# Optimization experiments

Hardware: AMD Instinct MI355X
Metric: run time of the kernel (lower is better)

The kernel has to match this reference:

```python
import jax, jax.numpy as jnp
import numpy as np

V, E, HT, HC = 30000, 300, 256, 256
B, LC, T = 32, 32, 64
NTAG = 9  # output_dim + 2


def lstm_dir(x, lens, Wih, Whh, b, reverse):
    """Variable-length single-direction LSTM (packed-sequence semantics).
    x: [N, T, D], lens: [N] int. Returns outputs [N, T, H] zeroed at pad steps.
    Masked state update keeps h,c frozen at pad steps, so reverse=True starts
    from each sequence's true last element (zeros carry through leading pads).
    """
    N, Tn, _ = x.shape
    H = Whh.shape[1]
    gx = jnp.einsum('ntd,gd->ntg', x, Wih) + b            # [N,T,4H]
    mask = jnp.arange(Tn)[None, :] < lens[:, None]         # [N,T]

    def step(carry, inp):
        h, c = carry
        g_t, m = inp                                       # [N,4H], [N]
        gates = g_t + h @ Whh.T
        i, f, g, o = jnp.split(gates, 4, axis=-1)
        c_new = jax.nn.sigmoid(f) * c + jax.nn.sigmoid(i) * jnp.tanh(g)
        h_new = jax.nn.sigmoid(o) * jnp.tanh(c_new)
        m = m[:, None]
        h2 = jnp.where(m, h_new, h)
        c2 = jnp.where(m, c_new, c)
        return (h2, c2), jnp.where(m, h2, 0.0)

    init = (jnp.zeros((N, H), x.dtype), jnp.zeros((N, H), x.dtype))
    xs = (jnp.swapaxes(gx, 0, 1), mask.T)
    _, ys = jax.lax.scan(step, init, xs, reverse=reverse)
    return jnp.swapaxes(ys, 0, 1)                          # [N,T,H]


def bilstm(x, lens, Wih_f, Whh_f, b_f, Wih_b, Whh_b, b_b):
    hf = lstm_dir(x, lens, Wih_f, Whh_f, b_f, reverse=False)
    hb = lstm_dir(x, lens, Wih_b, Whh_b, b_b, reverse=True)
    return jnp.concatenate([hf, hb], axis=-1)


def setup_inputs() -> dict:
    key = jax.random.key(0)
    ks = jax.random.split(key, 20)
    s = 0.05
    inp = {
        'x': jax.random.randint(ks[0], (B, LC, T), 0, V, dtype=jnp.int32),
        'x_feats': jax.random.normal(ks[1], (B, LC, 64), jnp.float32),
        'x_len': jnp.maximum(jax.random.randint(ks[2], (B,), 0, LC, dtype=jnp.int32), 1),
        'x_chunk_len': jax.random.randint(ks[3], (B, LC), 1, T + 1, dtype=jnp.int32),
        'emb': jax.random.normal(ks[4], (V, E), jnp.float32) * s,
        'tok_Wih_f': jax.random.normal(ks[5], (4 * HT, E), jnp.float32) * s,
        'tok_Whh_f': jax.random.normal(ks[6], (4 * HT, HT), jnp.float32) * s,
        'tok_b_f': jax.random.normal(ks[7], (4 * HT,), jnp.float32) * s,
        'tok_Wih_b': jax.random.normal(ks[8], (4 * HT, E), jnp.float32) * s,
        'tok_Whh_b': jax.random.normal(ks[9], (4 * HT, HT), jnp.float32) * s,
        'tok_b_b': jax.random.normal(ks[10], (4 * HT,), jnp.float32) * s,
        'chk_Wih_f': jax.random.normal(ks[11], (4 * HC, 2 * HT), jnp.float32) * s,
        'chk_Whh_f': jax.random.normal(ks[12], (4 * HC, HC), jnp.float32) * s,
        'chk_b_f': jax.random.normal(ks[13], (4 * HC,), jnp.float32) * s,
        'chk_Wih_b': jax.random.normal(ks[14], (4 * HC, 2 * HT), jnp.float32) * s,
        'chk_Whh_b': jax.random.normal(ks[15], (4 * HC, HC), jnp.float32) * s,
        'chk_b_b': jax.random.normal(ks[16], (4 * HC,), jnp.float32) * s,
        'fc_W': jax.random.normal(ks[17], (NTAG, 2 * HC), jnp.float32) * s,
        'fc_b': jax.random.normal(ks[18], (NTAG,), jnp.float32) * s,
    }
    return inp


def reference(x, x_feats, x_len, x_chunk_len, emb,
              tok_Wih_f, tok_Whh_f, tok_b_f, tok_Wih_b, tok_Whh_b, tok_b_b,
              chk_Wih_f, chk_Whh_f, chk_b_f, chk_Wih_b, chk_Whh_b, chk_b_b,
              fc_W, fc_b):
    b, lc, t = x.shape
    xe = emb[x].reshape(b * lc, t, -1)                     # [B*LC, T, E]
    clens = jnp.clip(x_chunk_len.reshape(-1), 1, t)        # [B*LC]
    h = bilstm(xe, clens, tok_Wih_f, tok_Whh_f, tok_b_f,
               tok_Wih_b, tok_Whh_b, tok_b_b)              # [B*LC, T, 2HT]
    # gather output at last valid timestep (= [fwd final, bwd one-step])
    last = h[jnp.arange(b * lc), clens - 1]                # [B*LC, 2HT]
    chunks = last.reshape(b, lc, -1)                       # [B, LC, 2HT]
    ch = bilstm(chunks, x_len, chk_Wih_f, chk_Whh_f, chk_b_f,
                chk_Wih_b, chk_Whh_b, chk_b_b)             # [B, LC, 2HC]
    # pad_packed(total_length=LC) gives zeros at pad -> fc sees zeros there
    out = ch @ fc_W.T + fc_b                               # [B, LC, NTAG]
    return out
```

## Files before the change

### kernel.cpp

```cpp
#include <hip/hip_runtime.h>


typedef __attribute__((ext_vector_type(8))) short s16x8;
typedef __attribute__((ext_vector_type(4))) float f32x4;
typedef __attribute__((ext_vector_type(2))) unsigned int u32x2;
typedef __attribute__((ext_vector_type(4))) unsigned int u32x4;

__device__ __forceinline__ unsigned short f2bf(float f) {
  unsigned u = __builtin_bit_cast(unsigned, f);
  u += 0x7fff + ((u >> 16) & 1);
  return (unsigned short)(u >> 16);
}
__device__ __forceinline__ float bf2f(unsigned short h) {
  unsigned u = ((unsigned)h) << 16;
  return __builtin_bit_cast(float, u);
}
__device__ __forceinline__ float sigm(float x) { return 1.f / (1.f + __expf(-x)); }
__device__ __forceinline__ float tanh_(float x) { return 1.f - 2.f / (__expf(2.f * x) + 1.f); }

union PK8 { s16x8 v; unsigned short u[8]; };

__global__ void prep_weights(const float* __restrict__ wihf, const float* __restrict__ wihb,
                             const float* __restrict__ wcf, const float* __restrict__ wcb,
                             unsigned short* __restrict__ o_wf, unsigned short* __restrict__ o_wb,
                             unsigned short* __restrict__ o_wcf, unsigned short* __restrict__ o_wcb) {
  const int job = blockIdx.y, r = blockIdx.x, tid = threadIdx.x;
  const float* src; unsigned short* dst; int Ks, Kd;
  switch (job) {
    case 0: src = wihf; dst = o_wf;   Ks = 300; Kd = 320; break;
    case 1: src = wihb; dst = o_wb;   Ks = 300; Kd = 320; break;
    case 2: src = wcf;  dst = o_wcf;  Ks = 512; Kd = 512; break;
    default:src = wcb;  dst = o_wcb;  Ks = 512; Kd = 512; break;
  }
  for (int c = tid; c < Kd; c += 256)
    dst[r * Kd + c] = f2bf(c < Ks ? src[r * Ks + c] : 0.f);
}

__global__ __launch_bounds__(256)
void prep_whh_frag(const float* __restrict__ w0, const float* __restrict__ w1,
                   const float* __restrict__ w2,
                   unsigned short* __restrict__ o0, unsigned short* __restrict__ o1,
                   unsigned short* __restrict__ o2) {
  const float* src = blockIdx.y == 0 ? w0 : (blockIdx.y == 1 ? w1 : w2);
  unsigned short* dst = blockIdx.y == 0 ? o0 : (blockIdx.y == 1 ? o1 : o2);
  const int fid = blockIdx.x;
  const int b = fid & 1, g = (fid >> 1) & 3, kt = (fid >> 3) & 7, js = fid >> 6;
  for (int i = threadIdx.x; i < 512; i += 256) {
    const int lane = i >> 3, e = i & 7;
    const int cc = lane & 15, qq = lane >> 4;
    const int row = g * 256 + (js * 2 + b) * 16 + cc;
    const int col = kt * 32 + qq * 8 + e;
    dst[(size_t)fid * 512 + i] = f2bf(src[row * 256 + col]);
  }
}

__global__ void prep_small(const int* __restrict__ x, const int* __restrict__ xcl,
                           int* __restrict__ clens, int* __restrict__ lastv,
                           int* __restrict__ order, int* __restrict__ glen) {
  __shared__ int start[65];
  const int n = threadIdx.x;
  if (n < 65) start[n] = 0;
  __syncthreads();
  int len = xcl[n]; len = len < 1 ? 1 : (len > 64 ? 64 : len);
  clens[n] = len;
  lastv[n] = x[n * 64 + len - 1];
  atomicAdd(&start[len], 1);
  __syncthreads();
  if (n == 0) {
    int acc = 0;
    for (int l = 64; l >= 1; --l) { int h = start[l]; start[l] = acc; acc += h; }
  }
  __syncthreads();
  int pos = atomicAdd(&start[len], 1);
  order[pos] = n;
  __syncthreads();
  if (n < 64) glen[n] = clens[order[n * 16]];
}

__global__ __launch_bounds__(256, 2)
void gemm_bf(const float* __restrict__ A, const int* __restrict__ rowmap,
             int Mrows, int Astride, int Klog, int KP,
             const unsigned short* __restrict__ B, unsigned short* __restrict__ C) {
  __shared__ unsigned short As[128 * 40];
  __shared__ unsigned short Ep[4][64 * 136];
  const int tid = threadIdx.x;
  const int lane = tid & 63, w = tid >> 6;
  const int wrow = w >> 1, wcol = w & 1;
  const int cc = lane & 15, qq = lane >> 4;
  const int m0 = blockIdx.y * 128, n0 = blockIdx.x * 256;

  f32x4 zz = {0.f, 0.f, 0.f, 0.f};
  f32x4 acc[4][8];
#pragma unroll
  for (int i = 0; i < 4; ++i)
#pragma unroll
    for (int j = 0; j < 8; ++j) acc[i][j] = zz;

  const int arow = tid >> 1, ahalf = tid & 1;
  const float* arp = nullptr;
  {
    int av = m0 + arow;
    if (av < Mrows) {
      int amap = rowmap ? rowmap[av] : av;
      arp = A + (long)amap * Astride;
    }
  }

  const int nktiles = KP >> 5;
  for (int kt = 0; kt < nktiles; ++kt) {
    const int k0 = kt << 5;
    __syncthreads();
    {
      const int kb = k0 + ahalf * 16;
      unsigned short hv[16];
      if (arp && kb + 16 <= Klog) {
        const float* p = arp + kb;
#pragma unroll
        for (int i = 0; i < 16; i += 4) {
          f32x4 t = *(const f32x4*)(p + i);
          hv[i] = f2bf(t.x); hv[i + 1] = f2bf(t.y);
          hv[i + 2] = f2bf(t.z); hv[i + 3] = f2bf(t.w);
        }
      } else {
#pragma unroll
        for (int i = 0; i < 16; ++i) {
          float v = (arp && (kb + i) < Klog) ? arp[kb + i] : 0.f;
          hv[i] = f2bf(v);
        }
      }
      PK8 p0, p1;
#pragma unroll
      for (int i = 0; i < 8; ++i) { p0.u[i] = hv[i]; p1.u[i] = hv[8 + i]; }
      *(s16x8*)&As[arow * 40 + ahalf * 16] = p0.v;
      *(s16x8*)&As[arow * 40 + ahalf * 16 + 8] = p1.v;
    }
    __syncthreads();
    s16x8 af[4];
#pragma unroll
    for (int mt = 0; mt < 4; ++mt)
      af[mt] = *(const s16x8*)&As[(wrow * 64 + mt * 16 + cc) * 40 + qq * 8];
#pragma unroll
    for (int nt = 0; nt < 8; ++nt) {
      const unsigned short* bp = B + (long)(n0 + wcol * 128 + nt * 16 + cc) * KP + k0 + qq * 8;
      s16x8 bfr = *(const s16x8*)bp;
#pragma unroll
      for (int mt = 0; mt < 4; ++mt)
        acc[mt][nt] = __builtin_amdgcn_mfma_f32_16x16x32_bf16(af[mt], bfr, acc[mt][nt], 0, 0, 0);
    }
  }
  __syncthreads();
#pragma unroll
  for (int mt = 0; mt < 4; ++mt)
#pragma unroll
    for (int nt = 0; nt < 8; ++nt)
#pragma unroll
      for (int r = 0; r < 4; ++r)
        Ep[w][(mt * 16 + qq * 4 + r) * 136 + nt * 16 + cc] = f2bf(acc[mt][nt][r]);
  __syncthreads();
#pragma unroll
  for (int it = 0; it < 16; ++it) {
    int row = it * 4 + qq;
    s16x8 d = *(const s16x8*)&Ep[w][row * 136 + cc * 8];
    int gm = m0 + wrow * 64 + row;
    int gn = n0 + wcol * 128 + cc * 8;
    if (gm < Mrows) *(s16x8*)&C[(long)gm * 1024 + gn] = d;
  }
}

__global__ void bwd_step(const unsigned short* __restrict__ gxb,
                         const float* __restrict__ bias,
                         float* __restrict__ chunks) {
  const int n = blockIdx.x, j = threadIdx.x;
  const unsigned short* row = gxb + (long)n * 1024;
  float gi = bf2f(row[j]) + bias[j];
  float gg = bf2f(row[512 + j]) + bias[512 + j];
  float go = bf2f(row[768 + j]) + bias[768 + j];
  float cn = sigm(gi) * tanh_(gg);
  chunks[(long)n * 512 + 256 + j] = sigm(go) * tanh_(cn);
}

__device__ __forceinline__ int gx_perm(int j) {
  return (j & ~31) + ((j & 15) << 1) + ((j >> 4) & 1);
}

__global__ __launch_bounds__(256)
void gather_gx(const unsigned short* __restrict__ proj, const int* __restrict__ x,
               const int* __restrict__ order, const int* __restrict__ clens,
               const int* __restrict__ glen, const float* __restrict__ bias,
               unsigned short* __restrict__ gx) {
  const int t = blockIdx.x, p = blockIdx.y, j = threadIdx.x;
  if (t >= glen[p >> 4]) return;
  const int seq = order[p];
  const int len = clens[seq];
  if (t >= len) return;
  unsigned short* dst = gx + (((size_t)(p >> 4) * 64 + t) * 16 + (p & 15)) * 1024 + gx_perm(j) * 4;
  const int tok = x[seq * 64 + t];
  const unsigned short* src = proj + (size_t)tok * 1024 + j;
  unsigned v0 = f2bf(bf2f(src[0]) + bias[j]);
  unsigned v1 = f2bf(bf2f(src[256]) + bias[256 + j]);
  unsigned v2 = f2bf(bf2f(src[512]) + bias[512 + j]);
  unsigned v3 = f2bf(bf2f(src[768]) + bias[768 + j]);
  u32x2 pk = {v0 | (v1 << 16), v2 | (v3 << 16)};
  *(u32x2*)dst = pk;
}

__global__ __launch_bounds__(256)
void repack4(const unsigned short* __restrict__ s0, const unsigned short* __restrict__ s1,
             const float* __restrict__ b0, const float* __restrict__ b1,
             unsigned short* __restrict__ d0, unsigned short* __restrict__ d1) {
  const int r = blockIdx.x, j = threadIdx.x;
  const int m = r >> 5, t = r & 31;
  const int mg = m >> 4, m16 = m & 15;
  const unsigned short* s = (blockIdx.y ? s1 : s0) + (size_t)r * 1024;
  const float* bb = blockIdx.y ? b1 : b0;
  unsigned short* d = (blockIdx.y ? d1 : d0) +
                      (size_t)((mg * 32 + t) * 16 + m16) * 1024 + gx_perm(j) * 4;
  unsigned v0 = f2bf(bf2f(s[j]) + bb[j]);
  unsigned v1 = f2bf(bf2f(s[256 + j]) + bb[256 + j]);
  unsigned v2 = f2bf(bf2f(s[512 + j]) + bb[512 + j]);
  unsigned v3 = f2bf(bf2f(s[768 + j]) + bb[768 + j]);
  u32x2 pk = {v0 | (v1 << 16), v2 | (v3 << 16)};
  *(u32x2*)d = pk;
}

__global__ __launch_bounds__(512, 2)
void tok_fwd(const unsigned short* __restrict__ gx,
             const unsigned short* __restrict__ WhP,
             const int* __restrict__ order,
             const int* __restrict__ clens,
             const int* __restrict__ glen,
             float* __restrict__ chunks) {
  extern __shared__ unsigned short smem[];
  unsigned short* hbuf = smem;
  unsigned short* ldsW = smem + 8448;
  int* sg = (int*)(smem + 8448 + 65536);
  int* slen = sg + 16;

  const int tid = threadIdx.x;
  const int lane = tid & 63, w = tid >> 6;
  const int cc = lane & 15, qq = lane >> 4;
  const int gb = blockIdx.x;

  if (tid < 16) {
    int s = order[gb * 16 + tid];
    sg[tid] = s;
    slen[tid] = clens[s];
  }
  for (int i = tid; i < 4224; i += 512) hbuf[i] = 0;

  const unsigned short* wgl = WhP + (size_t)w * 64 * 512 + lane * 8;
  {
    unsigned short* ld = ldsW + w * 8192 + lane * 8;
#pragma unroll
    for (int s = 0; s < 16; ++s)
      *(s16x8*)&ld[s * 512] = *(const s16x8*)&wgl[s * 512];
  }
  s16x8 Rw[40];
#pragma unroll
  for (int s = 0; s < 40; ++s)
    Rw[s] = *(const s16x8*)&wgl[(16 + s) * 512];

  __syncthreads();

  const int maxlen = glen[gb];
  int lenr[4];
#pragma unroll
  for (int r = 0; r < 4; ++r) lenr[r] = slen[qq * 4 + r];

  float cst[8];
  unsigned short hreg[8];
#pragma unroll
  for (int i = 0; i < 8; ++i) { cst[i] = 0.f; hreg[i] = 0; }

  const int j0 = w * 32 + cc;
  const unsigned short* gx0 = gx + (size_t)gb * 64 * 16 * 1024 + (w * 32 + cc * 2) * 4;
  const unsigned short* ldw = ldsW + w * 8192 + lane * 8;
  f32x4 zz = {0.f, 0.f, 0.f, 0.f};

  for (int t = 0; t < maxlen; ++t) {
    const unsigned short* hr = hbuf + (t & 1) * 4224;
    unsigned short* hw = hbuf + ((t & 1) ^ 1) * 4224;

    __syncthreads();

    s16x8 W7[4];
#pragma unroll
    for (int s = 0; s < 4; ++s)
      W7[s] = *(const s16x8*)&wgl[(56 + s) * 512];

    u32x4 gxp[4];
#pragma unroll
    for (int r = 0; r < 4; ++r)
      gxp[r] = *(const u32x4*)(gx0 + ((size_t)t * 16 + qq * 4 + r) * 1024);

    f32x4 acc[8];
#pragma unroll
    for (int s = 0; s < 8; ++s) acc[s] = zz;

#pragma unroll
    for (int kt = 0; kt < 2; ++kt) {
      s16x8 a0 = *(const s16x8*)&hr[cc * 264 + kt * 32 + qq * 8];
#pragma unroll
      for (int s = 0; s < 8; ++s)
        acc[s] = __builtin_amdgcn_mfma_f32_16x16x32_bf16(
            a0, *(const s16x8*)&ldw[(kt * 8 + s) * 512], acc[s], 0, 0, 0);
    }
#pragma unroll
    for (int kt = 2; kt < 7; ++kt) {
      s16x8 a0 = *(const s16x8*)&hr[cc * 264 + kt * 32 + qq * 8];
#pragma unroll
      for (int s = 0; s < 8; ++s)
        acc[s] = __builtin_amdgcn_mfma_f32_16x16x32_bf16(
            a0, Rw[(kt - 2) * 8 + s], acc[s], 0, 0, 0);
    }
    {
      s16x8 a7 = *(const s16x8*)&hr[cc * 264 + 7 * 32 + qq * 8];
#pragma unroll
      for (int s = 0; s < 4; ++s)
        acc[s] = __builtin_amdgcn_mfma_f32_16x16x32_bf16(a7, W7[s], acc[s], 0, 0, 0);
#pragma unroll
      for (int s = 0; s < 4; ++s)
        W7[s] = *(const s16x8*)&wgl[(60 + s) * 512];
#pragma unroll
      for (int s = 0; s < 4; ++s)
        acc[4 + s] = __builtin_amdgcn_mfma_f32_16x16x32_bf16(a7, W7[s], acc[4 + s], 0, 0, 0);
    }

#pragma unroll
    for (int r = 0; r < 4; ++r) {
      const int m = qq * 4 + r;
      const bool upd = t < lenr[r];
      const u32x4 pk = gxp[r];
#pragma unroll
      for (int jj = 0; jj < 2; ++jj) {
        const unsigned lo = jj ? pk.z : pk.x;
        const unsigned hi = jj ? pk.w : pk.y;
        float gi = acc[0 * 2 + jj][r] + bf2f((unsigned short)(lo & 0xffff));
        float gf = acc[1 * 2 + jj][r] + bf2f((unsigned short)(lo >> 16));
        float gg = acc[2 * 2 + jj][r] + bf2f((unsigned short)(hi & 0xffff));
        float go = acc[3 * 2 + jj][r] + bf2f((unsigned short)(hi >> 16));
        const int si = r * 2 + jj;
        if (upd) {
          float cn = sigm(gf) * cst[si] + sigm(gi) * tanh_(gg);
          cst[si] = cn;
          hreg[si] = f2bf(sigm(go) * tanh_(cn));
        }
        hw[m * 264 + j0 + jj * 16] = hreg[si];
      }
    }
  }

#pragma unroll
  for (int r = 0; r < 4; ++r)
#pragma unroll
    for (int jj = 0; jj < 2; ++jj)
      chunks[(size_t)sg[qq * 4 + r] * 512 + j0 + jj * 16] = bf2f(hreg[r * 2 + jj]);
}

__global__ __launch_bounds__(512, 2)
void chunk_rec(const unsigned short* __restrict__ gxf,
               const unsigned short* __restrict__ gxb,
               const unsigned short* __restrict__ WhPf,
               const unsigned short* __restrict__ WhPb,
               const int* __restrict__ xlen,
               unsigned short* __restrict__ ch) {
  extern __shared__ unsigned short smem[];
  unsigned short* hbuf = smem;
  unsigned short* ldsW = smem + 8448;

  const int tid = threadIdx.x;
  const int lane = tid & 63, w = tid >> 6;
  const int cc = lane & 15, qq = lane >> 4;
  const int dir = blockIdx.x & 1, mg = blockIdx.x >> 1;
  const unsigned short* gx = (dir ? gxb : gxf) + (size_t)mg * 32 * 16 * 1024
                             + (w * 32 + cc * 2) * 4;
  const unsigned short* WhP = dir ? WhPb : WhPf;

  for (int i = tid; i < 4224; i += 512) hbuf[i] = 0;

  const unsigned short* wgl = WhP + (size_t)w * 64 * 512 + lane * 8;
  {
    unsigned short* ld = ldsW + w * 8192 + lane * 8;
#pragma unroll
    for (int s = 0; s < 16; ++s)
      *(s16x8*)&ld[s * 512] = *(const s16x8*)&wgl[s * 512];
  }
  s16x8 Rw[40];
#pragma unroll
  for (int s = 0; s < 40; ++s)
    Rw[s] = *(const s16x8*)&wgl[(16 + s) * 512];

  __syncthreads();

  const int j0 = w * 32 + cc;
  int lenr[4];
#pragma unroll
  for (int r = 0; r < 4; ++r) {
    int L = xlen[mg * 16 + qq * 4 + r];
    lenr[r] = L > 32 ? 32 : L;
  }

  float cst[8];
  unsigned short hreg[8];
#pragma unroll
  for (int i = 0; i < 8; ++i) { cst[i] = 0.f; hreg[i] = 0; }

  const unsigned short* ldw = ldsW + w * 8192 + lane * 8;
  f32x4 zz = {0.f, 0.f, 0.f, 0.f};

  for (int tt = 0; tt < 32; ++tt) {
    const int t = dir ? (31 - tt) : tt;
    const unsigned short* hr = hbuf + (tt & 1) * 4224;
    unsigned short* hw = hbuf + ((tt & 1) ^ 1) * 4224;

    __syncthreads();

    s16x8 W7[4];
#pragma unroll
    for (int s = 0; s < 4; ++s)
      W7[s] = *(const s16x8*)&wgl[(56 + s) * 512];

    u32x4 gxp[4];
#pragma unroll
    for (int r = 0; r < 4; ++r)
      gxp[r] = *(const u32x4*)(gx + ((size_t)t * 16 + qq * 4 + r) * 1024);

    f32x4 acc[8];
#pragma unroll
    for (int s = 0; s < 8; ++s) acc[s] = zz;

#pragma unroll
    for (int kt = 0; kt < 2; ++kt) {
      s16x8 a0 = *(const s16x8*)&hr[cc * 264 + kt * 32 + qq * 8];
#pragma unroll
      for (int s = 0; s < 8; ++s)
        acc[s] = __builtin_amdgcn_mfma_f32_16x16x32_bf16(
            a0, *(const s16x8*)&ldw[(kt * 8 + s) * 512], acc[s], 0, 0, 0);
    }
#pragma unroll
    for (int kt = 2; kt < 7; ++kt) {
      s16x8 a0 = *(const s16x8*)&hr[cc * 264 + kt * 32 + qq * 8];
#pragma unroll
      for (int s = 0; s < 8; ++s)
        acc[s] = __builtin_amdgcn_mfma_f32_16x16x32_bf16(
            a0, Rw[(kt - 2) * 8 + s], acc[s], 0, 0, 0);
    }
    {
      s16x8 a7 = *(const s16x8*)&hr[cc * 264 + 7 * 32 + qq * 8];
#pragma unroll
      for (int s = 0; s < 4; ++s)
        acc[s] = __builtin_amdgcn_mfma_f32_16x16x32_bf16(a7, W7[s], acc[s], 0, 0, 0);
#pragma unroll
      for (int s = 0; s < 4; ++s)
        W7[s] = *(const s16x8*)&wgl[(60 + s) * 512];
#pragma unroll
      for (int s = 0; s < 4; ++s)
        acc[4 + s] = __builtin_amdgcn_mfma_f32_16x16x32_bf16(a7, W7[s], acc[4 + s], 0, 0, 0);
    }

#pragma unroll
    for (int r = 0; r < 4; ++r) {
      const int m = qq * 4 + r;
      const bool upd = t < lenr[r];
      const u32x4 pk = gxp[r];
#pragma unroll
      for (int jj = 0; jj < 2; ++jj) {
        const unsigned lo = jj ? pk.z : pk.x;
        const unsigned hi = jj ? pk.w : pk.y;
        float gi = acc[0 * 2 + jj][r] + bf2f((unsigned short)(lo & 0xffff));
        float gf = acc[1 * 2 + jj][r] + bf2f((unsigned short)(lo >> 16));
        float gg = acc[2 * 2 + jj][r] + bf2f((unsigned short)(hi & 0xffff));
        float go = acc[3 * 2 + jj][r] + bf2f((unsigned short)(hi >> 16));
        const int si = r * 2 + jj;
        unsigned short out16 = 0;
        if (upd) {
          float cn = sigm(gf) * cst[si] + sigm(gi) * tanh_(gg);
          cst[si] = cn;
          hreg[si] = f2bf(sigm(go) * tanh_(cn));
          out16 = hreg[si];
        }
        hw[m * 264 + j0 + jj * 16] = hreg[si];
        ch[(size_t)((mg * 16 + m) * 32 + t) * 512 + dir * 256 + j0 + jj * 16] = out16;
      }
    }
  }
}

__global__ __launch_bounds__(64)
void fc_kernel(const unsigned short* __restrict__ ch, const float* __restrict__ W,
               const float* __restrict__ bfc, float* __restrict__ out) {
  const int n = blockIdx.x, lane = threadIdx.x;
  float xv[8];
  const unsigned short* cp = ch + (long)n * 512 + lane * 8;
#pragma unroll
  for (int i = 0; i < 8; ++i) xv[i] = bf2f(cp[i]);
  float s[9];
#pragma unroll
  for (int k = 0; k < 9; ++k) {
    const float* wr = W + k * 512 + lane * 8;
    float t = 0.f;
#pragma unroll
    for (int i = 0; i < 8; ++i) t += xv[i] * wr[i];
    s[k] = t;
  }
#pragma unroll
  for (int off = 32; off; off >>= 1)
#pragma unroll
    for (int k = 0; k < 9; ++k) s[k] += __shfl_down(s[k], off, 64);
  if (lane == 0) {
#pragma unroll
    for (int k = 0; k < 9; ++k) out[n * 9 + k] = s[k] + bfc[k];
  }
}

extern "C" void kernel_launch(void* const* d_in, const int* in_sizes, int n_in,
                              void* d_out, int out_size, void* d_ws, size_t ws_size,
                              hipStream_t stream) {
  const int*   x           = (const int*)d_in[0];
  const int*   x_len       = (const int*)d_in[2];
  const int*   x_chunk_len = (const int*)d_in[3];
  const float* emb         = (const float*)d_in[4];
  const float* tok_Wih_f   = (const float*)d_in[5];
  const float* tok_Whh_f   = (const float*)d_in[6];
  const float* tok_b_f     = (const float*)d_in[7];
  const float* tok_Wih_b   = (const float*)d_in[8];
  const float* tok_b_b     = (const float*)d_in[10];
  const float* chk_Wih_f   = (const float*)d_in[11];
  const float* chk_Whh_f   = (const float*)d_in[12];
  const float* chk_b_f     = (const float*)d_in[13];
  const float* chk_Wih_b   = (const float*)d_in[14];
  const float* chk_Whh_b   = (const float*)d_in[15];
  const float* chk_b_b     = (const float*)d_in[16];
  const float* fc_W        = (const float*)d_in[17];
  const float* fc_b        = (const float*)d_in[18];
  float* out = (float*)d_out;

  char* ws = (char*)d_ws;
  size_t off = 0;
  auto alloc = [&](size_t bytes) -> void* {
    void* p = ws + off;
    off += (bytes + 255) & ~(size_t)255;
    return p;
  };
  unsigned short* Wf   = (unsigned short*)alloc((size_t)1024 * 320 * 2);
  unsigned short* Wb   = (unsigned short*)alloc((size_t)1024 * 320 * 2);
  unsigned short* Wcf  = (unsigned short*)alloc((size_t)1024 * 512 * 2);
  unsigned short* Wcb  = (unsigned short*)alloc((size_t)1024 * 512 * 2);
  unsigned short* WhPtok=(unsigned short*)alloc((size_t)512 * 512 * 2);
  unsigned short* WhPcf= (unsigned short*)alloc((size_t)512 * 512 * 2);
  unsigned short* WhPcb= (unsigned short*)alloc((size_t)512 * 512 * 2);
  unsigned short* proj = (unsigned short*)alloc((size_t)30000 * 1024 * 2);
  unsigned short* gxbb = (unsigned short*)alloc((size_t)1024 * 1024 * 2);
  unsigned short* gxcf = (unsigned short*)alloc((size_t)1024 * 1024 * 2);
  unsigned short* gxcb = (unsigned short*)alloc((size_t)1024 * 1024 * 2);
  unsigned short* gxcfp= (unsigned short*)alloc((size_t)1024 * 1024 * 2);
  unsigned short* gxcbp= (unsigned short*)alloc((size_t)1024 * 1024 * 2);
  float*          chunks = (float*)alloc((size_t)1024 * 512 * 4);
  unsigned short* cho  = (unsigned short*)alloc((size_t)1024 * 512 * 2);
  unsigned short* gxs  = (unsigned short*)alloc((size_t)1024 * 64 * 1024 * 2);
  int* clens = (int*)alloc(1024 * 4);
  int* lastv = (int*)alloc(1024 * 4);
  int* order = (int*)alloc(1024 * 4);
  int* glen  = (int*)alloc(64 * 4);

  hipFuncSetAttribute((const void*)tok_fwd,
                      hipFuncAttributeMaxDynamicSharedMemorySize, 148096);
  hipFuncSetAttribute((const void*)chunk_rec,
                      hipFuncAttributeMaxDynamicSharedMemorySize, 147968);

  prep_weights<<<dim3(1024, 4), 256, 0, stream>>>(
      tok_Wih_f, tok_Wih_b, chk_Wih_f, chk_Wih_b, Wf, Wb, Wcf, Wcb);
  prep_whh_frag<<<dim3(512, 3), 256, 0, stream>>>(
      tok_Whh_f, chk_Whh_f, chk_Whh_b, WhPtok, WhPcf, WhPcb);
  prep_small<<<1, 1024, 0, stream>>>(x, x_chunk_len, clens, lastv, order, glen);

  gemm_bf<<<dim3(4, 235), 256, 0, stream>>>(emb, nullptr, 30000, 300, 300, 320, Wf, proj);
  gemm_bf<<<dim3(4, 8), 256, 0, stream>>>(emb, lastv, 1024, 300, 300, 320, Wb, gxbb);
  bwd_step<<<1024, 256, 0, stream>>>(gxbb, tok_b_b, chunks);
  gather_gx<<<dim3(64, 1024), 256, 0, stream>>>(proj, x, order, clens, glen, tok_b_f, gxs);
  tok_fwd<<<64, 512, 148096, stream>>>(gxs, WhPtok, order, clens, glen, chunks);
  gemm_bf<<<dim3(4, 8), 256, 0, stream>>>(chunks, nullptr, 1024, 512, 512, 512, Wcf, gxcf);
  gemm_bf<<<dim3(4, 8), 256, 0, stream>>>(chunks, nullptr, 1024, 512, 512, 512, Wcb, gxcb);
  repack4<<<dim3(1024, 2), 256, 0, stream>>>(gxcf, gxcb, chk_b_f, chk_b_b, gxcfp, gxcbp);
  chunk_rec<<<4, 512, 147968, stream>>>(gxcfp, gxcbp, WhPcf, WhPcb, x_len, cho);
  fc_kernel<<<1024, 64, 0, stream>>>(cho, fc_W, fc_b, out);
}
```

Before: 798.4 us.

## Prefetch streamed weights and gate inputs across steps and use lighter LDS barrier

Both recurrent kernels now keep 32 weight slices resident in registers instead of 40, and stream the remaining 16 slices (48..63) from global memory. The first batch of streamed slices and the next step's gate inputs are issued at the end of the previous step so their latency overlaps the barrier and the LDS reads. The per-step __syncthreads is replaced by an explicit lgkmcnt wait plus s_barrier bracketed by sched_barriers, so outstanding global loads are not drained at the barrier. The occupancy hint moves to amdgpu_waves_per_eu(2,2). The cost is more global weight traffic per step and tighter control over the scheduler.

```diff
diff --git a/kernel.cpp b/kernel.cpp
--- a/kernel.cpp
+++ b/kernel.cpp
@@ -17,6 +17,13 @@
 }
 __device__ __forceinline__ float sigm(float x) { return 1.f / (1.f + __expf(-x)); }
 __device__ __forceinline__ float tanh_(float x) { return 1.f - 2.f / (__expf(2.f * x) + 1.f); }
+
+__device__ __forceinline__ void lds_barrier() {
+  __builtin_amdgcn_sched_barrier(0);
+  asm volatile("s_waitcnt lgkmcnt(0)" ::: "memory");
+  __builtin_amdgcn_s_barrier();
+  __builtin_amdgcn_sched_barrier(0);
+}
 
 union PK8 { s16x8 v; unsigned short u[8]; };
 
@@ -223,7 +230,7 @@
   *(u32x2*)d = pk;
 }
 
-__global__ __launch_bounds__(512, 2)
+__global__ __launch_bounds__(512) __attribute__((amdgpu_waves_per_eu(2, 2)))
 void tok_fwd(const unsigned short* __restrict__ gx,
              const unsigned short* __restrict__ WhP,
              const int* __restrict__ order,
@@ -246,7 +253,7 @@
     sg[tid] = s;
     slen[tid] = clens[s];
   }
-  for (int i = tid; i < 4224; i += 512) hbuf[i] = 0;
+  for (int i = tid; i < 8448; i += 512) hbuf[i] = 0;
 
   const unsigned short* wgl = WhP + (size_t)w * 64 * 512 + lane * 8;
   {
@@ -255,9 +262,9 @@
     for (int s = 0; s < 16; ++s)
       *(s16x8*)&ld[s * 512] = *(const s16x8*)&wgl[s * 512];
   }
-  s16x8 Rw[40];
-#pragma unroll
-  for (int s = 0; s < 40; ++s)
+  s16x8 Rw[32];
+#pragma unroll
+  for (int s = 0; s < 32; ++s)
     Rw[s] = *(const s16x8*)&wgl[(16 + s) * 512];
 
   __syncthreads();
@@ -277,21 +284,20 @@
   const unsigned short* ldw = ldsW + w * 8192 + lane * 8;
   f32x4 zz = {0.f, 0.f, 0.f, 0.f};
 
+  s16x8 S[8];
+#pragma unroll
+  for (int s = 0; s < 8; ++s)
+    S[s] = *(const s16x8*)&wgl[(48 + s) * 512];
+  u32x4 gxp[4];
+#pragma unroll
+  for (int r = 0; r < 4; ++r)
+    gxp[r] = *(const u32x4*)(gx0 + ((size_t)qq * 4 + r) * 1024);
+
   for (int t = 0; t < maxlen; ++t) {
     const unsigned short* hr = hbuf + (t & 1) * 4224;
     unsigned short* hw = hbuf + ((t & 1) ^ 1) * 4224;
 
-    __syncthreads();
-
-    s16x8 W7[4];
-#pragma unroll
-    for (int s = 0; s < 4; ++s)
-      W7[s] = *(const s16x8*)&wgl[(56 + s) * 512];
-
-    u32x4 gxp[4];
-#pragma unroll
-    for (int r = 0; r < 4; ++r)
-      gxp[r] = *(const u32x4*)(gx0 + ((size_t)t * 16 + qq * 4 + r) * 1024);
+    lds_barrier();
 
     f32x4 acc[8];
 #pragma unroll
@@ -306,7 +312,7 @@
             a0, *(const s16x8*)&ldw[(kt * 8 + s) * 512], acc[s], 0, 0, 0);
     }
 #pragma unroll
-    for (int kt = 2; kt < 7; ++kt) {
+    for (int kt = 2; kt < 6; ++kt) {
       s16x8 a0 = *(const s16x8*)&hr[cc * 264 + kt * 32 + qq * 8];
 #pragma unroll
       for (int s = 0; s < 8; ++s)
@@ -314,16 +320,19 @@
             a0, Rw[(kt - 2) * 8 + s], acc[s], 0, 0, 0);
     }
     {
+      s16x8 a6 = *(const s16x8*)&hr[cc * 264 + 6 * 32 + qq * 8];
+#pragma unroll
+      for (int s = 0; s < 8; ++s)
+        acc[s] = __builtin_amdgcn_mfma_f32_16x16x32_bf16(a6, S[s], acc[s], 0, 0, 0);
+    }
+#pragma unroll
+    for (int s = 0; s < 8; ++s)
+      S[s] = *(const s16x8*)&wgl[(56 + s) * 512];
+    {
       s16x8 a7 = *(const s16x8*)&hr[cc * 264 + 7 * 32 + qq * 8];
 #pragma unroll
-      for (int s = 0; s < 4; ++s)
-        acc[s] = __builtin_amdgcn_mfma_f32_16x16x32_bf16(a7, W7[s], acc[s], 0, 0, 0);
-#pragma unroll
-      for (int s = 0; s < 4; ++s)
-        W7[s] = *(const s16x8*)&wgl[(60 + s) * 512];
-#pragma unroll
-      for (int s = 0; s < 4; ++s)
-        acc[4 + s] = __builtin_amdgcn_mfma_f32_16x16x32_bf16(a7, W7[s], acc[4 + s], 0, 0, 0);
+      for (int s = 0; s < 8; ++s)
+        acc[s] = __builtin_amdgcn_mfma_f32_16x16x32_bf16(a7, S[s], acc[s], 0, 0, 0);
     }
 
 #pragma unroll
@@ -348,6 +357,14 @@
         hw[m * 264 + j0 + jj * 16] = hreg[si];
       }
     }
+
+#pragma unroll
+    for (int s = 0; s < 8; ++s)
+      S[s] = *(const s16x8*)&wgl[(48 + s) * 512];
+    const int tn = (t + 1 < maxlen) ? t + 1 : t;
+#pragma unroll
+    for (int r = 0; r < 4; ++r)
+      gxp[r] = *(const u32x4*)(gx0 + ((size_t)tn * 16 + qq * 4 + r) * 1024);
   }
 
 #pragma unroll
@@ -357,7 +374,7 @@
       chunks[(size_t)sg[qq * 4 + r] * 512 + j0 + jj * 16] = bf2f(hreg[r * 2 + jj]);
 }
 
-__global__ __launch_bounds__(512, 2)
+__global__ __launch_bounds__(512) __attribute__((amdgpu_waves_per_eu(2, 2)))
 void chunk_rec(const unsigned short* __restrict__ gxf,
                const unsigned short* __restrict__ gxb,
                const unsigned short* __restrict__ WhPf,
@@ -376,7 +393,7 @@
                              + (w * 32 + cc * 2) * 4;
   const unsigned short* WhP = dir ? WhPb : WhPf;
 
-  for (int i = tid; i < 4224; i += 512) hbuf[i] = 0;
+  for (int i = tid; i < 8448; i += 512) hbuf[i] = 0;
 
   const unsigned short* wgl = WhP + (size_t)w * 64 * 512 + lane * 8;
   {
@@ -385,9 +402,9 @@
     for (int s = 0; s < 16; ++s)
       *(s16x8*)&ld[s * 512] = *(const s16x8*)&wgl[s * 512];
   }
-  s16x8 Rw[40];
-#pragma unroll
-  for (int s = 0; s < 40; ++s)
+  s16x8 Rw[32];
+#pragma unroll
+  for (int s = 0; s < 32; ++s)
     Rw[s] = *(const s16x8*)&wgl[(16 + s) * 512];
 
   __syncthreads();
@@ -407,23 +424,23 @@
 
   const unsigned short* ldw = ldsW + w * 8192 + lane * 8;
   f32x4 zz = {0.f, 0.f, 0.f, 0.f};
+
+  s16x8 S[8];
+#pragma unroll
+  for (int s = 0; s < 8; ++s)
+    S[s] = *(const s16x8*)&wgl[(48 + s) * 512];
+  const int t0 = dir ? 31 : 0;
+  u32x4 gxp[4];
+#pragma unroll
+  for (int r = 0; r < 4; ++r)
+    gxp[r] = *(const u32x4*)(gx + ((size_t)t0 * 16 + qq * 4 + r) * 1024);
 
   for (int tt = 0; tt < 32; ++tt) {
     const int t = dir ? (31 - tt) : tt;
     const unsigned short* hr = hbuf + (tt & 1) * 4224;
     unsigned short* hw = hbuf + ((tt & 1) ^ 1) * 4224;
 
-    __syncthreads();
-
-    s16x8 W7[4];
-#pragma unroll
-    for (int s = 0; s < 4; ++s)
-      W7[s] = *(const s16x8*)&wgl[(56 + s) * 512];
-
-    u32x4 gxp[4];
-#pragma unroll
-    for (int r = 0; r < 4; ++r)
-      gxp[r] = *(const u32x4*)(gx + ((size_t)t * 16 + qq * 4 + r) * 1024);
+    lds_barrier();
 
     f32x4 acc[8];
 #pragma unroll
@@ -438,7 +455,7 @@
             a0, *(const s16x8*)&ldw[(kt * 8 + s) * 512], acc[s], 0, 0, 0);
     }
 #pragma unroll
-    for (int kt = 2; kt < 7; ++kt) {
+    for (int kt = 2; kt < 6; ++kt) {
       s16x8 a0 = *(const s16x8*)&hr[cc * 264 + kt * 32 + qq * 8];
 #pragma unroll
       for (int s = 0; s < 8; ++s)
@@ -446,16 +463,19 @@
             a0, Rw[(kt - 2) * 8 + s], acc[s], 0, 0, 0);
     }
     {
+      s16x8 a6 = *(const s16x8*)&hr[cc * 264 + 6 * 32 + qq * 8];
+#pragma unroll
+      for (int s = 0; s < 8; ++s)
+        acc[s] = __builtin_amdgcn_mfma_f32_16x16x32_bf16(a6, S[s], acc[s], 0, 0, 0);
+    }
+#pragma unroll
+    for (int s = 0; s < 8; ++s)
+      S[s] = *(const s16x8*)&wgl[(56 + s) * 512];
+    {
       s16x8 a7 = *(const s16x8*)&hr[cc * 264 + 7 * 32 + qq * 8];
 #pragma unroll
-      for (int s = 0; s < 4; ++s)
-        acc[s] = __builtin_amdgcn_mfma_f32_16x16x32_bf16(a7, W7[s], acc[s], 0, 0, 0);
-#pragma unroll
-      for (int s = 0; s < 4; ++s)
-        W7[s] = *(const s16x8*)&wgl[(60 + s) * 512];
-#pragma unroll
-      for (int s = 0; s < 4; ++s)
-        acc[4 + s] = __builtin_amdgcn_mfma_f32_16x16x32_bf16(a7, W7[s], acc[4 + s], 0, 0, 0);
+      for (int s = 0; s < 8; ++s)
+        acc[s] = __builtin_amdgcn_mfma_f32_16x16x32_bf16(a7, S[s], acc[s], 0, 0, 0);
     }
 
 #pragma unroll
@@ -483,6 +503,15 @@
         ch[(size_t)((mg * 16 + m) * 32 + t) * 512 + dir * 256 + j0 + jj * 16] = out16;
       }
     }
+
+#pragma unroll
+    for (int s = 0; s < 8; ++s)
+      S[s] = *(const s16x8*)&wgl[(48 + s) * 512];
+    const int ttn = (tt + 1 < 32) ? tt + 1 : tt;
+    const int tn = dir ? (31 - ttn) : ttn;
+#pragma unroll
+    for (int r = 0; r < 4; ++r)
+      gxp[r] = *(const u32x4*)(gx + ((size_t)tn * 16 + qq * 4 + r) * 1024);
   }
 }
 
```

After: 857.6 us. 7.4% more time.
